# Kernel tuning notes

Hardware: AMD Instinct MI355X
Metric: run time of the kernel (lower is better)

Reference implementation:

```python
import jax, jax.numpy as jnp
import numpy as np

N_NODES = 50000
N_EDGES = 1_600_000
IN_CH, HID_CH, OUT_CH, EDGE_DIM = 128, 128, 64, 16
NEG_SLOPE = 0.2


def _glorot(key, shape):
    fan = sum(shape) if len(shape) > 1 else shape[0] + 1
    lim = jnp.sqrt(6.0 / fan)
    return jax.random.uniform(key, shape, jnp.float32, -lim, lim)


def setup_inputs() -> dict:
    key = jax.random.key(0)
    ks = jax.random.split(key, 16)
    x = jax.random.normal(ks[0], (N_NODES, IN_CH), jnp.float32)
    edge_index = jax.random.randint(ks[1], (2, N_EDGES), 0, N_NODES, jnp.int32)
    flepe = jax.random.normal(ks[2], (N_EDGES, EDGE_DIM), jnp.float32)
    # layer 1 params (GATConv heads=1)
    W1 = _glorot(ks[3], (IN_CH, HID_CH))
    att_src1 = _glorot(ks[4], (HID_CH,))
    att_dst1 = _glorot(ks[5], (HID_CH,))
    We1 = _glorot(ks[6], (EDGE_DIM, HID_CH))
    att_edge1 = _glorot(ks[7], (HID_CH,))
    b1 = jnp.zeros((HID_CH,), jnp.float32)
    # layer 2 params
    W2 = _glorot(ks[8], (HID_CH, OUT_CH))
    att_src2 = _glorot(ks[9], (OUT_CH,))
    att_dst2 = _glorot(ks[10], (OUT_CH,))
    We2 = _glorot(ks[11], (EDGE_DIM, OUT_CH))
    att_edge2 = _glorot(ks[12], (OUT_CH,))
    b2 = jnp.zeros((OUT_CH,), jnp.float32)
    return {"x": x, "edge_index": edge_index, "flepe": flepe,
            "W1": W1, "att_src1": att_src1, "att_dst1": att_dst1,
            "We1": We1, "att_edge1": att_edge1, "b1": b1,
            "W2": W2, "att_src2": att_src2, "att_dst2": att_dst2,
            "We2": We2, "att_edge2": att_edge2, "b2": b2}


def gat_conv(x, src, dst, edge_attr, W, a_s, a_d, We, a_e, b, n_nodes):
    # PyG GATConv, heads=1, concat=True, negative_slope=0.2, edge_dim set.
    h = x @ W                                    # [N, C]
    alpha_src = h @ a_s                          # [N]
    alpha_dst = h @ a_d                          # [N]
    e = edge_attr @ We                           # [E, C]
    alpha_edge = e @ a_e                         # [E]
    alpha = alpha_src[src] + alpha_dst[dst] + alpha_edge
    alpha = jax.nn.leaky_relu(alpha, NEG_SLOPE)  # [E]
    # segment softmax over incoming edges per destination node
    amax = jax.ops.segment_max(alpha, dst, num_segments=n_nodes)
    amax = jnp.where(jnp.isfinite(amax), amax, 0.0)
    ex = jnp.exp(alpha - amax[dst])
    denom = jax.ops.segment_sum(ex, dst, num_segments=n_nodes)
    coef = ex / (denom[dst] + 1e-16)
    out = jax.ops.segment_sum(coef[:, None] * h[src], dst, num_segments=n_nodes)
    return out + b


def reference(x, edge_index, flepe,
              W1, att_src1, att_dst1, We1, att_edge1, b1,
              W2, att_src2, att_dst2, We2, att_edge2, b2):
    src, dst = edge_index[0], edge_index[1]
    n = x.shape[0]
    # dropout(p=0.5) is identity in eval mode
    h = gat_conv(x, src, dst, flepe, W1, att_src1, att_dst1, We1, att_edge1, b1, n)
    h = jax.nn.relu(h)
    out = gat_conv(h, src, dst, flepe, W2, att_src2, att_dst2, We2, att_edge2, b2, n)
    return out
```

## Files before the change

### kernel.cpp

```cpp
#include <hip/hip_runtime.h>
#include <hip/hip_bf16.h>

typedef unsigned int uint;
typedef __attribute__((ext_vector_type(8))) short bf16x8;
typedef __attribute__((ext_vector_type(4))) float f32x4;


__device__ inline float bf2f_lo(uint u) { return __uint_as_float((u & 0xffffu) << 16); }
__device__ inline float bf2f_hi(uint u) { return __uint_as_float(u & 0xffff0000u); }
__device__ inline uint f2bf_rne(float f) {
    uint x = __float_as_uint(f);
    return (x + 0x7fffu + ((x >> 16) & 1u)) >> 16;
}
__device__ inline uint pack_bf2(float a, float b) { return f2bf_rne(a) | (f2bf_rne(b) << 16); }

__global__ void k_prep(const float* __restrict__ W1, const float* __restrict__ W2,
                       uint4* __restrict__ S1, uint4* __restrict__ S2) {
    int t = blockIdx.x * 256 + threadIdx.x;
    if (t < 2048) {
        int f = t >> 6, l = t & 63;
        int kb = f >> 3, cb = f & 7;
        int k0 = kb * 32 + (l >> 4) * 8, c = cb * 16 + (l & 15);
        uint u[4];
#pragma unroll
        for (int m = 0; m < 4; ++m)
            u[m] = pack_bf2(W1[(k0 + 2 * m) * 128 + c], W1[(k0 + 2 * m + 1) * 128 + c]);
        S1[t] = make_uint4(u[0], u[1], u[2], u[3]);
    } else if (t < 3072) {
        int tt = t - 2048;
        int f = tt >> 6, l = tt & 63;
        int kb = f >> 2, cb = f & 3;
        int k0 = kb * 32 + (l >> 4) * 8, c = cb * 16 + (l & 15);
        uint u[4];
#pragma unroll
        for (int m = 0; m < 4; ++m)
            u[m] = pack_bf2(W2[(k0 + 2 * m) * 64 + c], W2[(k0 + 2 * m + 1) * 64 + c]);
        S2[tt] = make_uint4(u[0], u[1], u[2], u[3]);
    }
}

__global__ void k_deg(const int* __restrict__ dst, int* __restrict__ deg, int E,
                      const float* __restrict__ We1, const float* __restrict__ ae1w,
                      const float* __restrict__ We2, const float* __restrict__ ae2w,
                      float* __restrict__ p1, float* __restrict__ p2) {
    if (blockIdx.x == 0) {
        int t = threadIdx.x;
        if (t < 16) {
            float s = 0.f;
            for (int c = 0; c < 128; ++c) s += We1[t * 128 + c] * ae1w[c];
            p1[t] = s;
        } else if (t < 32) {
            int d = t - 16;
            float s = 0.f;
            for (int c = 0; c < 64; ++c) s += We2[d * 64 + c] * ae2w[c];
            p2[d] = s;
        }
    }
    int e = blockIdx.x * blockDim.x + threadIdx.x;
    if (e < E) atomicAdd(&deg[dst[e]], 1);
}

__global__ __launch_bounds__(1024) void k_scanA(const int* __restrict__ deg,
                                                int* __restrict__ excl,
                                                int* __restrict__ bsum, int N) {
    __shared__ int s[1024];
    int tid = threadIdx.x;
    int gid = blockIdx.x * 1024 + tid;
    int v = (gid < N) ? deg[gid] : 0;
    s[tid] = v;
    __syncthreads();
    for (int off = 1; off < 1024; off <<= 1) {
        int t = (tid >= off) ? s[tid - off] : 0;
        __syncthreads();
        s[tid] += t;
        __syncthreads();
    }
    if (gid < N) excl[gid] = s[tid] - v;
    if (tid == 1023) bsum[blockIdx.x] = s[1023];
}

__global__ void k_scanB(const int* __restrict__ bsum, int* __restrict__ bsumx, int nb,
                        int* __restrict__ rowstart, int N, int E) {
    int t = threadIdx.x;
    int v = (t < nb) ? bsum[t] : 0;
    int x = v;
    for (int o = 1; o < 64; o <<= 1) {
        int y = __shfl_up(x, o);
        if (t >= o) x += y;
    }
    if (t < nb) bsumx[t] = x - v;
    if (t == 0) rowstart[N] = E;
}

__global__ __launch_bounds__(1024) void k_scanC(const int* __restrict__ excl,
                                                const int* __restrict__ bsumx,
                                                int* __restrict__ rowstart,
                                                int* __restrict__ cursor, int N) {
    int gid = blockIdx.x * 1024 + threadIdx.x;
    if (gid < N) {
        int v = excl[gid] + bsumx[blockIdx.x];
        rowstart[gid] = v;
        cursor[gid] = v;
    }
}

__global__ void k_scat(const int* __restrict__ src, const int* __restrict__ dst,
                       const float* __restrict__ fe,
                       const float* __restrict__ p1, const float* __restrict__ p2,
                       int* __restrict__ cursor, f32x4* __restrict__ rec, int E) {
    float q1[16], q2[16];
#pragma unroll
    for (int i = 0; i < 16; ++i) { q1[i] = p1[i]; q2[i] = p2[i]; }
    int e = blockIdx.x * blockDim.x + threadIdx.x;
    if (e >= E) return;
    int s = src[e], d = dst[e];
    int pos = atomicAdd(&cursor[d], 1);
    const float4* f = reinterpret_cast<const float4*>(fe) + (size_t)e * 4;
    float a1 = 0.f, a2 = 0.f;
#pragma unroll
    for (int j = 0; j < 4; ++j) {
        float4 v = f[j];
        a1 += v.x * q1[4 * j] + v.y * q1[4 * j + 1] + v.z * q1[4 * j + 2] + v.w * q1[4 * j + 3];
        a2 += v.x * q2[4 * j] + v.y * q2[4 * j + 1] + v.z * q2[4 * j + 2] + v.w * q2[4 * j + 3];
    }
    f32x4 r = {__int_as_float(s), a1, a2, 0.f};
    __builtin_nontemporal_store(r, rec + pos);
}

template <int COUT, bool BF16IN>
__global__ __launch_bounds__(256) void k_gemm_mfma(
    const void* __restrict__ Xv, const uint4* __restrict__ Wswz,
    const float* __restrict__ avs, const float* __restrict__ avd,
    uint* __restrict__ Hb, float* __restrict__ asrc, float* __restrict__ adst,
    int ntiles) {
    constexpr int NCB = COUT / 16;
    constexpr int NFRAG = NCB * 4;
    __shared__ uint4 WB[NFRAG * 64];
    for (int i = threadIdx.x; i < NFRAG * 64; i += 256) WB[i] = Wswz[i];
    __syncthreads();
    const int wv = threadIdx.x >> 6, l = threadIdx.x & 63;
    const int lrow = l & 15, lkq = l >> 4;

    float vs[NCB], vd[NCB];
#pragma unroll
    for (int cb = 0; cb < NCB; ++cb) {
        vs[cb] = avs[cb * 16 + lrow];
        vd[cb] = avd[cb * 16 + lrow];
    }
    union U16 { uint4 q; bf16x8 v; };

    for (int t = blockIdx.x * 4 + wv; t < ntiles; t += gridDim.x * 4) {
        const int rowb = t * 16;
        const int r0 = rowb + lrow;
        bf16x8 a[4];
        if constexpr (BF16IN) {
            const uint4* xr4 = reinterpret_cast<const uint4*>(Xv) + (size_t)r0 * 16;
#pragma unroll
            for (int kb = 0; kb < 4; ++kb) {
                U16 cv; cv.q = xr4[kb * 4 + lkq];
                a[kb] = cv.v;
            }
        } else {
            const float* xr = reinterpret_cast<const float*>(Xv) + (size_t)r0 * 128 + lkq * 8;
#pragma unroll
            for (int kb = 0; kb < 4; ++kb) {
                float4 f0 = *reinterpret_cast<const float4*>(xr + kb * 32);
                float4 f1 = *reinterpret_cast<const float4*>(xr + kb * 32 + 4);
                U16 cv;
                cv.q = make_uint4(pack_bf2(f0.x, f0.y), pack_bf2(f0.z, f0.w),
                                  pack_bf2(f1.x, f1.y), pack_bf2(f1.z, f1.w));
                a[kb] = cv.v;
            }
        }
        f32x4 acc[NCB];
#pragma unroll
        for (int cb = 0; cb < NCB; ++cb) acc[cb] = (f32x4){0.f, 0.f, 0.f, 0.f};
#pragma unroll
        for (int cb = 0; cb < NCB; ++cb) {
#pragma unroll
            for (int kb = 0; kb < 4; ++kb) {
                U16 bu;
                bu.q = WB[(kb * NCB + cb) * 64 + l];
                acc[cb] = __builtin_amdgcn_mfma_f32_16x16x32_bf16(a[kb], bu.v, acc[cb], 0, 0, 0);
            }
        }
        float ps[4] = {0.f, 0.f, 0.f, 0.f}, pd[4] = {0.f, 0.f, 0.f, 0.f};
#pragma unroll
        for (int cb = 0; cb < NCB; ++cb) {
#pragma unroll
            for (int r = 0; r < 4; ++r) {
                float v = acc[cb][r];
                ps[r] += v * vs[cb];
                pd[r] += v * vd[cb];
                float pv = __shfl_xor(v, 1);
                if (!(l & 1))
                    Hb[(size_t)(rowb + lkq * 4 + r) * (COUT / 2) + cb * 8 + (lrow >> 1)] =
                        pack_bf2(v, pv);
            }
        }
#pragma unroll
        for (int o = 1; o < 16; o <<= 1) {
#pragma unroll
            for (int r = 0; r < 4; ++r) {
                ps[r] += __shfl_xor(ps[r], o);
                pd[r] += __shfl_xor(pd[r], o);
            }
        }
        if (lrow == 0) {
            int rb = rowb + lkq * 4;
#pragma unroll
            for (int r = 0; r < 4; ++r) { asrc[rb + r] = ps[r]; adst[rb + r] = pd[r]; }
        }
    }
}

__global__ __launch_bounds__(256) void k_aggr1(
    const int* __restrict__ rowstart, const float4* __restrict__ rec,
    const float* __restrict__ asrc, const float* __restrict__ adst,
    const uint4* __restrict__ H4, const float* __restrict__ bias,
    uint4* __restrict__ out4, int N) {
    __shared__ uint2 swl[4][64];
    const int wv = threadIdx.x >> 6, lane = threadIdx.x & 63;
    const int eg = lane >> 4, ch = lane & 15;
    int n = blockIdx.x * 4 + wv;
    if (n >= N) return;
    n = __builtin_amdgcn_readfirstlane(n);
    int s = rowstart[n], e = rowstart[n + 1];
    float ad = adst[n];
    float acc[8];
#pragma unroll
    for (int k = 0; k < 8; ++k) acc[k] = 0.f;
    float ws = 0.f;
    for (int base = s; base < e; base += 64) {
        int cnt = e - base; if (cnt > 64) cnt = 64;
        float w = 0.f; int sn = 0;
        if (lane < cnt) {
            float4 rc = rec[base + lane];
            sn = __float_as_int(rc.x);
            float al = asrc[sn] + ad + rc.y;
            al = al > 0.f ? al : 0.2f * al;
            w = __expf(al);
        }
        float wsum = w;
        for (int o = 32; o; o >>= 1) wsum += __shfl_xor(wsum, o);
        ws += wsum;
        swl[wv][lane] = make_uint2((uint)sn, __float_as_uint(w));
        int cnt4 = (cnt + 3) & ~3;
        for (int j = 0; j < cnt4; j += 4) {
            uint2 t = swl[wv][j + eg];
            float w0 = __uint_as_float(t.y);
            uint4 h = H4[(size_t)t.x * 16 + ch];
            acc[0] = fmaf(w0, bf2f_lo(h.x), acc[0]); acc[1] = fmaf(w0, bf2f_hi(h.x), acc[1]);
            acc[2] = fmaf(w0, bf2f_lo(h.y), acc[2]); acc[3] = fmaf(w0, bf2f_hi(h.y), acc[3]);
            acc[4] = fmaf(w0, bf2f_lo(h.z), acc[4]); acc[5] = fmaf(w0, bf2f_hi(h.z), acc[5]);
            acc[6] = fmaf(w0, bf2f_lo(h.w), acc[6]); acc[7] = fmaf(w0, bf2f_hi(h.w), acc[7]);
        }
    }
#pragma unroll
    for (int o = 16; o <= 32; o <<= 1)
#pragma unroll
        for (int k = 0; k < 8; ++k) acc[k] += __shfl_xor(acc[k], o);
    if (eg == 0) {
        float inv = 1.0f / (ws + 1e-16f);
        float4 b0 = reinterpret_cast<const float4*>(bias)[ch * 2];
        float4 b1 = reinterpret_cast<const float4*>(bias)[ch * 2 + 1];
        float o0 = fmaxf(fmaf(acc[0], inv, b0.x), 0.f);
        float o1 = fmaxf(fmaf(acc[1], inv, b0.y), 0.f);
        float o2 = fmaxf(fmaf(acc[2], inv, b0.z), 0.f);
        float o3 = fmaxf(fmaf(acc[3], inv, b0.w), 0.f);
        float o4 = fmaxf(fmaf(acc[4], inv, b1.x), 0.f);
        float o5 = fmaxf(fmaf(acc[5], inv, b1.y), 0.f);
        float o6 = fmaxf(fmaf(acc[6], inv, b1.z), 0.f);
        float o7 = fmaxf(fmaf(acc[7], inv, b1.w), 0.f);
        out4[(size_t)n * 16 + ch] = make_uint4(pack_bf2(o0, o1), pack_bf2(o2, o3),
                                               pack_bf2(o4, o5), pack_bf2(o6, o7));
    }
}

__global__ __launch_bounds__(256) void k_aggr2(
    const int* __restrict__ rowstart, const float4* __restrict__ rec,
    const float* __restrict__ asrc, const float* __restrict__ adst,
    const uint4* __restrict__ H4, const float* __restrict__ bias,
    float* __restrict__ out, int N) {
    __shared__ uint2 swl[4][64];
    const int wv = threadIdx.x >> 6, lane = threadIdx.x & 63;
    const int eg = lane >> 3, ch = lane & 7;
    int n = blockIdx.x * 4 + wv;
    if (n >= N) return;
    n = __builtin_amdgcn_readfirstlane(n);
    int s = rowstart[n], e = rowstart[n + 1];
    float ad = adst[n];
    float acc[8];
#pragma unroll
    for (int k = 0; k < 8; ++k) acc[k] = 0.f;
    float ws = 0.f;
    for (int base = s; base < e; base += 64) {
        int cnt = e - base; if (cnt > 64) cnt = 64;
        float w = 0.f; int sn = 0;
        if (lane < cnt) {
            float4 rc = rec[base + lane];
            sn = __float_as_int(rc.x);
            float al = asrc[sn] + ad + rc.z;
            al = al > 0.f ? al : 0.2f * al;
            w = __expf(al);
        }
        float wsum = w;
        for (int o = 32; o; o >>= 1) wsum += __shfl_xor(wsum, o);
        ws += wsum;
        swl[wv][lane] = make_uint2((uint)sn, __float_as_uint(w));
        int cnt8 = (cnt + 7) & ~7;
        for (int j = 0; j < cnt8; j += 8) {
            uint2 t = swl[wv][j + eg];
            float w0 = __uint_as_float(t.y);
            uint4 h = H4[(size_t)t.x * 8 + ch];
            acc[0] = fmaf(w0, bf2f_lo(h.x), acc[0]); acc[1] = fmaf(w0, bf2f_hi(h.x), acc[1]);
            acc[2] = fmaf(w0, bf2f_lo(h.y), acc[2]); acc[3] = fmaf(w0, bf2f_hi(h.y), acc[3]);
            acc[4] = fmaf(w0, bf2f_lo(h.z), acc[4]); acc[5] = fmaf(w0, bf2f_hi(h.z), acc[5]);
            acc[6] = fmaf(w0, bf2f_lo(h.w), acc[6]); acc[7] = fmaf(w0, bf2f_hi(h.w), acc[7]);
        }
    }
#pragma unroll
    for (int o = 8; o <= 32; o <<= 1)
#pragma unroll
        for (int k = 0; k < 8; ++k) acc[k] += __shfl_xor(acc[k], o);
    if (eg == 0) {
        float inv = 1.0f / (ws + 1e-16f);
        float4 b0 = reinterpret_cast<const float4*>(bias)[ch * 2];
        float4 b1 = reinterpret_cast<const float4*>(bias)[ch * 2 + 1];
        float4 o0 = make_float4(fmaf(acc[0], inv, b0.x), fmaf(acc[1], inv, b0.y),
                                fmaf(acc[2], inv, b0.z), fmaf(acc[3], inv, b0.w));
        float4 o1 = make_float4(fmaf(acc[4], inv, b1.x), fmaf(acc[5], inv, b1.y),
                                fmaf(acc[6], inv, b1.z), fmaf(acc[7], inv, b1.w));
        float4* op = reinterpret_cast<float4*>(out + (size_t)n * 64 + ch * 8);
        op[0] = o0;
        op[1] = o1;
    }
}

extern "C" void kernel_launch(void* const* d_in, const int* in_sizes, int n_in,
                              void* d_out, int out_size, void* d_ws, size_t ws_size,
                              hipStream_t stream) {
    const float* x    = (const float*)d_in[0];
    const int*   ei   = (const int*)d_in[1];
    const float* fe   = (const float*)d_in[2];
    const float* W1   = (const float*)d_in[3];
    const float* as1  = (const float*)d_in[4];
    const float* ad1  = (const float*)d_in[5];
    const float* We1  = (const float*)d_in[6];
    const float* ae1w = (const float*)d_in[7];
    const float* b1   = (const float*)d_in[8];
    const float* W2   = (const float*)d_in[9];
    const float* as2  = (const float*)d_in[10];
    const float* ad2  = (const float*)d_in[11];
    const float* We2  = (const float*)d_in[12];
    const float* ae2w = (const float*)d_in[13];
    const float* b2   = (const float*)d_in[14];
    float* out = (float*)d_out;

    const int N = in_sizes[0] / 128;
    const int E = in_sizes[1] / 2;
    const int* src = ei;
    const int* dst = ei + E;

    char* ws = (char*)d_ws;
    size_t off = 0;
    auto alloc = [&](size_t bytes) -> void* {
        void* p = ws + off;
        off = (off + bytes + 255) & ~(size_t)255;
        return p;
    };
    float*  p1       = (float*)alloc(64);
    float*  p2       = (float*)alloc(64);
    uint4*  S1       = (uint4*)alloc(2048 * 16);
    uint4*  S2       = (uint4*)alloc(1024 * 16);
    float4* rec      = (float4*)alloc((size_t)E * 16);
    uint*   x2       = (uint*)alloc((size_t)N * 64 * 4);
    uint*   H1       = (uint*)alloc((size_t)N * 64 * 4);
    uint*   H2       = (uint*)alloc((size_t)N * 32 * 4);
    float*  asrc     = (float*)alloc((size_t)N * 4);
    float*  adst     = (float*)alloc((size_t)N * 4);
    int*    deg      = (int*)alloc((size_t)N * 4);
    int*    excl     = (int*)alloc((size_t)N * 4);
    int*    rowstart = (int*)alloc((size_t)(N + 1) * 4);
    int*    cursor   = (int*)alloc((size_t)N * 4);
    int*    bsum     = (int*)alloc(256);
    int*    bsumx    = (int*)alloc(256);

    const int nb = (N + 1023) / 1024;
    const int ntiles = (N + 15) / 16;

    hipMemsetAsync(deg, 0, (size_t)N * 4, stream);
    k_prep<<<12, 256, 0, stream>>>(W1, W2, S1, S2);
    k_deg<<<(E + 255) / 256, 256, 0, stream>>>(dst, deg, E, We1, ae1w, We2, ae2w, p1, p2);
    k_scanA<<<nb, 1024, 0, stream>>>(deg, excl, bsum, N);
    k_scanB<<<1, 64, 0, stream>>>(bsum, bsumx, nb, rowstart, N, E);
    k_scanC<<<nb, 1024, 0, stream>>>(excl, bsumx, rowstart, cursor, N);
    k_scat<<<(E + 255) / 256, 256, 0, stream>>>(src, dst, fe, p1, p2, cursor,
                                                (f32x4*)rec, E);

    k_gemm_mfma<128, false><<<512, 256, 0, stream>>>(x, S1, as1, ad1, H1, asrc, adst, ntiles);
    k_aggr1<<<(N + 3) / 4, 256, 0, stream>>>(rowstart, rec, asrc, adst,
                                             (const uint4*)H1, b1, (uint4*)x2, N);

    k_gemm_mfma<64, true><<<512, 256, 0, stream>>>(x2, S2, as2, ad2, H2, asrc, adst, ntiles);
    k_aggr2<<<(N + 3) / 4, 256, 0, stream>>>(rowstart, rec, asrc, adst,
                                             (const uint4*)H2, b2, out, N);
}
```

Before: 462.5 us.

## Store per-edge data in edge order and gather via CSR edge-id permutation

The scatter kernel now writes per-edge records (src, edge attention) coalesced in original edge order, split into separate arrays per layer. It also writes a CSR permutation of edge ids, replacing the scattered 16-byte record write. The aggregation kernels then gather through the edge-id indirection. This swaps a random wide write for a random 4-byte write, at the cost of an extra dependent random 8-byte read per edge in each aggregation pass.

```diff
diff --git a/kernel.cpp b/kernel.cpp
--- a/kernel.cpp
+++ b/kernel.cpp
@@ -107,14 +107,14 @@
 __global__ void k_scat(const int* __restrict__ src, const int* __restrict__ dst,
                        const float* __restrict__ fe,
                        const float* __restrict__ p1, const float* __restrict__ p2,
-                       int* __restrict__ cursor, f32x4* __restrict__ rec, int E) {
+                       int* __restrict__ cursor, uint2* __restrict__ es1,
+                       uint2* __restrict__ es2, int* __restrict__ csr_eid, int E) {
     float q1[16], q2[16];
 #pragma unroll
     for (int i = 0; i < 16; ++i) { q1[i] = p1[i]; q2[i] = p2[i]; }
     int e = blockIdx.x * blockDim.x + threadIdx.x;
     if (e >= E) return;
     int s = src[e], d = dst[e];
-    int pos = atomicAdd(&cursor[d], 1);
     const float4* f = reinterpret_cast<const float4*>(fe) + (size_t)e * 4;
     float a1 = 0.f, a2 = 0.f;
 #pragma unroll
@@ -123,8 +123,10 @@
         a1 += v.x * q1[4 * j] + v.y * q1[4 * j + 1] + v.z * q1[4 * j + 2] + v.w * q1[4 * j + 3];
         a2 += v.x * q2[4 * j] + v.y * q2[4 * j + 1] + v.z * q2[4 * j + 2] + v.w * q2[4 * j + 3];
     }
-    f32x4 r = {__int_as_float(s), a1, a2, 0.f};
-    __builtin_nontemporal_store(r, rec + pos);
+    es1[e] = make_uint2((uint)s, __float_as_uint(a1));
+    es2[e] = make_uint2((uint)s, __float_as_uint(a2));
+    int pos = atomicAdd(&cursor[d], 1);
+    csr_eid[pos] = e;
 }
 
 template <int COUT, bool BF16IN>
@@ -215,7 +217,8 @@
 }
 
 __global__ __launch_bounds__(256) void k_aggr1(
-    const int* __restrict__ rowstart, const float4* __restrict__ rec,
+    const int* __restrict__ rowstart, const int* __restrict__ csr_eid,
+    const uint2* __restrict__ es1,
     const float* __restrict__ asrc, const float* __restrict__ adst,
     const uint4* __restrict__ H4, const float* __restrict__ bias,
     uint4* __restrict__ out4, int N) {
@@ -233,18 +236,19 @@
     float ws = 0.f;
     for (int base = s; base < e; base += 64) {
         int cnt = e - base; if (cnt > 64) cnt = 64;
-        float w = 0.f; int sn = 0;
+        float w = 0.f; uint sn = 0;
         if (lane < cnt) {
-            float4 rc = rec[base + lane];
-            sn = __float_as_int(rc.x);
-            float al = asrc[sn] + ad + rc.y;
+            int eid = csr_eid[base + lane];
+            uint2 es = es1[eid];
+            sn = es.x;
+            float al = asrc[sn] + ad + __uint_as_float(es.y);
             al = al > 0.f ? al : 0.2f * al;
             w = __expf(al);
         }
         float wsum = w;
         for (int o = 32; o; o >>= 1) wsum += __shfl_xor(wsum, o);
         ws += wsum;
-        swl[wv][lane] = make_uint2((uint)sn, __float_as_uint(w));
+        swl[wv][lane] = make_uint2(sn, __float_as_uint(w));
         int cnt4 = (cnt + 3) & ~3;
         for (int j = 0; j < cnt4; j += 4) {
             uint2 t = swl[wv][j + eg];
@@ -278,7 +282,8 @@
 }
 
 __global__ __launch_bounds__(256) void k_aggr2(
-    const int* __restrict__ rowstart, const float4* __restrict__ rec,
+    const int* __restrict__ rowstart, const int* __restrict__ csr_eid,
+    const uint2* __restrict__ es2,
     const float* __restrict__ asrc, const float* __restrict__ adst,
     const uint4* __restrict__ H4, const float* __restrict__ bias,
     float* __restrict__ out, int N) {
@@ -296,18 +301,19 @@
     float ws = 0.f;
     for (int base = s; base < e; base += 64) {
         int cnt = e - base; if (cnt > 64) cnt = 64;
-        float w = 0.f; int sn = 0;
+        float w = 0.f; uint sn = 0;
         if (lane < cnt) {
-            float4 rc = rec[base + lane];
-            sn = __float_as_int(rc.x);
-            float al = asrc[sn] + ad + rc.z;
+            int eid = csr_eid[base + lane];
+            uint2 es = es2[eid];
+            sn = es.x;
+            float al = asrc[sn] + ad + __uint_as_float(es.y);
             al = al > 0.f ? al : 0.2f * al;
             w = __expf(al);
         }
         float wsum = w;
         for (int o = 32; o; o >>= 1) wsum += __shfl_xor(wsum, o);
         ws += wsum;
-        swl[wv][lane] = make_uint2((uint)sn, __float_as_uint(w));
+        swl[wv][lane] = make_uint2(sn, __float_as_uint(w));
         int cnt8 = (cnt + 7) & ~7;
         for (int j = 0; j < cnt8; j += 8) {
             uint2 t = swl[wv][j + eg];
@@ -373,7 +379,9 @@
     float*  p2       = (float*)alloc(64);
     uint4*  S1       = (uint4*)alloc(2048 * 16);
     uint4*  S2       = (uint4*)alloc(1024 * 16);
-    float4* rec      = (float4*)alloc((size_t)E * 16);
+    uint2*  es1      = (uint2*)alloc((size_t)E * 8);
+    uint2*  es2      = (uint2*)alloc((size_t)E * 8);
+    int*    csr_eid  = (int*)alloc((size_t)E * 4);
     uint*   x2       = (uint*)alloc((size_t)N * 64 * 4);
     uint*   H1       = (uint*)alloc((size_t)N * 64 * 4);
     uint*   H2       = (uint*)alloc((size_t)N * 32 * 4);
@@ -396,13 +404,13 @@
     k_scanB<<<1, 64, 0, stream>>>(bsum, bsumx, nb, rowstart, N, E);
     k_scanC<<<nb, 1024, 0, stream>>>(excl, bsumx, rowstart, cursor, N);
     k_scat<<<(E + 255) / 256, 256, 0, stream>>>(src, dst, fe, p1, p2, cursor,
-                                                (f32x4*)rec, E);
+                                                es1, es2, csr_eid, E);
 
     k_gemm_mfma<128, false><<<512, 256, 0, stream>>>(x, S1, as1, ad1, H1, asrc, adst, ntiles);
-    k_aggr1<<<(N + 3) / 4, 256, 0, stream>>>(rowstart, rec, asrc, adst,
+    k_aggr1<<<(N + 3) / 4, 256, 0, stream>>>(rowstart, csr_eid, es1, asrc, adst,
                                              (const uint4*)H1, b1, (uint4*)x2, N);
 
     k_gemm_mfma<64, true><<<512, 256, 0, stream>>>(x2, S2, as2, ad2, H2, asrc, adst, ntiles);
-    k_aggr2<<<(N + 3) / 4, 256, 0, stream>>>(rowstart, rec, asrc, adst,
+    k_aggr2<<<(N + 3) / 4, 256, 0, stream>>>(rowstart, csr_eid, es2, asrc, adst,
                                              (const uint4*)H2, b2, out, N);
 }
```

Measured after the change: 471.4 us. No clear change (+1.9%).
